# Kernel optimization log

Hardware: AMD Instinct MI355X
Metric: run time of the kernel (lower is better)

Reference implementation:

```python
import jax, jax.numpy as jnp
import numpy as np

ITE = 20
LAM = 0.1
MU1_0 = 0.1
MU2_0 = 0.1
RHO = 1.05


def _shrink(x, t):
    # soft-threshold: sign(x) * max(|x| - t, 0)
    return jnp.sign(x) * jnp.maximum(jnp.abs(x) - t, 0.0)


# circular forward differences (kernel [1, -1]) along W, H, and spectral (C) axes
def _diff_h(x):
    return x - jnp.roll(x, -1, axis=-1)

def _diff_v(x):
    return x - jnp.roll(x, -1, axis=-2)

def _diff_s(x):
    return x - jnp.roll(x, -1, axis=1)

# adjoint (transpose) differences used inside the FFT-based TV solve
def _diff_hT(x):
    return x - jnp.roll(x, 1, axis=-1)

def _diff_vT(x):
    return x - jnp.roll(x, 1, axis=-2)

def _diff_sT(x):
    return x - jnp.roll(x, 1, axis=1)


def _demo(C, H, W):
    # |F(Dh)|^2 + |F(Dv)|^2 + |F(Ds)|^2 for circular [1,-1] kernels:
    # |1 - exp(-2*pi*i*k/L)|^2 = 2 - 2*cos(2*pi*k/L) along each axis.
    dc = 2.0 - 2.0 * jnp.cos(2.0 * jnp.pi * jnp.arange(C) / C)
    dh = 2.0 - 2.0 * jnp.cos(2.0 * jnp.pi * jnp.arange(H) / H)
    dw = 2.0 - 2.0 * jnp.cos(2.0 * jnp.pi * jnp.arange(W) / W)
    return (dc[:, None, None] + dh[None, :, None] + dw[None, None, :]).astype(jnp.float32)  # [C,H,W]


def _hwtv3d(Y, inW):
    N, C, H, W = Y.shape
    demo = _demo(C, H, W)  # [C,H,W], broadcasts over batch
    mu1, mu2, lam = MU1_0, MU2_0, LAM
    zero = jnp.float32(0.0)
    G1 = G21 = G22 = G23 = zero  # scalar zeros, broadcast like the torch `0`
    Z = Y
    X = Y
    DhZ, DvZ, DsZ = _diff_h(Z), _diff_v(Z), _diff_s(Z)
    for _ in range(ITE):
        Uh = _shrink(DhZ - G21 / mu2, lam / mu2)
        Uv = _shrink(DvZ - G22 / mu2, lam / mu2)
        Us = _shrink(DsZ - G23 / mu2, lam / mu2)
        # TV_solver3D: (mu1*I + mu2*(Dh^T Dh + Dv^T Dv + Ds^T Ds))^{-1} applied via 3D FFT
        numer = mu1 * (X + G1 / mu1) + mu2 * (
            _diff_hT(Uh + G21 / mu2) + _diff_vT(Uv + G22 / mu2) + _diff_sT(Us + G23 / mu2)
        )
        F = jnp.fft.fftn(numer, axes=(1, 2, 3))
        Z = jnp.real(jnp.fft.ifftn(F / (mu1 + mu2 * demo), axes=(1, 2, 3)))
        DhZ, DvZ, DsZ = _diff_h(Z), _diff_v(Z), _diff_s(Z)
        X = (inW * Y + mu1 * Z - G1) / (inW + mu1)
        G1 = G1 + mu1 * (X - Z)
        G21 = G21 + mu2 * (Uh - DhZ)
        G22 = G22 + mu2 * (Uv - DvZ)
        G23 = G23 + mu2 * (Us - DsZ)
        mu1 = RHO * mu1
        mu2 = RHO * mu2
    return Z


def setup_inputs() -> dict:
    key = jax.random.key(0)
    k1, k2 = jax.random.split(key)
    Y = jax.random.normal(k1, (4, 31, 128, 128), dtype=jnp.float32)
    inW = jax.random.uniform(k2, (4, 31, 128, 128), dtype=jnp.float32)
    return {"Y": Y, "inW": inW}


def reference(Y, inW):
    return _hwtv3d(Y, inW)
```

## Files before the change

### kernel.cpp

```cpp
#include <hip/hip_runtime.h>
#include <hip/hip_fp16.h>
#include <math.h>

#define N_ 4
#define C_ 31
#define H_ 128
#define W_ 128
#define TOTAL (N_*C_*H_*W_)
#define CV_ (C_*H_*W_)
#define PI_F 3.14159265358979f
#define RHO_F 1.05f
#define INV_RHO (1.0f/1.05f)
#define NORM2 (1.0f/16384.0f)

typedef __attribute__((ext_vector_type(2))) float v2f;
typedef __attribute__((ext_vector_type(2))) _Float16 h2f;

__device__ __forceinline__ v2f cmulv(v2f a, v2f b){
  v2f t = a.x * b;
  v2f s = (v2f){-a.y, a.y};
  return t + s * b.yx;
}
__device__ __forceinline__ v2f shflv(v2f v, int m){
  v2f r; r.x = __shfl_xor(v.x, m, 64); r.y = __shfl_xor(v.y, m, 64); return r;
}
__device__ __forceinline__ h2f shflh(h2f v, int m){
  float f = __builtin_bit_cast(float, v);
  f = __shfl_xor(f, m, 64);
  return __builtin_bit_cast(h2f, f);
}
__device__ __forceinline__ float shrinkf(float x, float t){
  return copysignf(fmaxf(fabsf(x) - t, 0.0f), x);
}
__device__ __forceinline__ uint packh2(v2f v){
  union{__half2 h2; uint u;} cv; cv.h2 = __floats2half2_rn(v.x, v.y); return cv.u;
}
__device__ __forceinline__ v2f unpackh2(uint u){
  union{uint uu; __half2 h2;} cv; cv.uu = u;
  float2 f = __half22float2(cv.h2);
  return (v2f){f.x, f.y};
}
__device__ __forceinline__ v2f h2v(__half2 h){
  float2 f = __half22float2(h);
  return (v2f){f.x, f.y};
}
__device__ __forceinline__ v2f vupd(v2f D, v2f vo, float thr){
  const float aa = 1.0f + INV_RHO;
  return (v2f){
    shrinkf(aa*D.x - vo.x*INV_RHO, thr) + (vo.x - D.x)*INV_RHO,
    shrinkf(aa*D.y - vo.y*INV_RHO, thr) + (vo.y - D.y)*INV_RHO};
}
__device__ __forceinline__ void load_tw(const v2f* __restrict__ lut, v2f* tw, int lane){
  #pragma unroll
  for (int i = 0; i < 7; ++i) tw[i] = lut[i*64 + lane];
}

__device__ __forceinline__ void fft128_fwd(v2f& a, v2f& b, const v2f* twf, int t){
  v2f u = a + b;
  v2f v = cmulv(a - b, twf[0]);
  #pragma unroll
  for (int i = 1; i < 7; ++i){
    int sp = 64 >> i;
    bool up = (t & sp) != 0;
    v2f pu = shflv(u, sp);
    v2f du = up ? pu - u : u + pu;
    u = cmulv(du, twf[i]);
    v2f pv = shflv(v, sp);
    v2f dv = up ? pv - v : v + pv;
    v = cmulv(dv, twf[i]);
  }
  a = u; b = v;
}

__device__ __forceinline__ void fft128_inv(v2f& a, v2f& b, const v2f* twi, int t){
  v2f u = a, v = b;
  #pragma unroll
  for (int i = 6; i >= 1; --i){
    int sp = 64 >> i;
    bool up = (t & sp) != 0;
    v2f pu = shflv(u, sp);
    v2f e  = up ? pu : u;
    v2f o  = up ? u  : pu;
    v2f wo = cmulv(o, twi[i]);
    u = up ? e - wo : e + wo;
    v2f pv = shflv(v, sp);
    v2f ev = up ? pv : v;
    v2f ov = up ? v  : pv;
    v2f wv = cmulv(ov, twi[i]);
    v = up ? ev - wv : ev + wv;
  }
  v2f tv = cmulv(v, twi[0]);
  a = u + tv;
  b = u - tv;
}

__device__ __forceinline__ void fft128_inv_h2(h2f& are, h2f& aim, h2f& bre, h2f& bim,
    const uint* __restrict__ twc, const uint* __restrict__ tws, int t){
  #pragma unroll
  for (int i = 6; i >= 1; --i){
    int sp = 64 >> i;
    bool up = (t & sp) != 0;
    h2f c2 = __builtin_bit_cast(h2f, twc[i*64 + t]);
    h2f s2 = __builtin_bit_cast(h2f, tws[i*64 + t]);
    h2f pre = shflh(are, sp), pim = shflh(aim, sp);
    h2f e_re = up ? pre : are, e_im = up ? pim : aim;
    h2f o_re = up ? are : pre, o_im = up ? aim : pim;
    are = e_re + (o_re*c2 - o_im*s2);
    aim = e_im + (o_re*s2 + o_im*c2);
    pre = shflh(bre, sp); pim = shflh(bim, sp);
    e_re = up ? pre : bre; e_im = up ? pim : bim;
    o_re = up ? bre : pre; o_im = up ? bim : pim;
    bre = e_re + (o_re*c2 - o_im*s2);
    bim = e_im + (o_re*s2 + o_im*c2);
  }
  h2f c0 = __builtin_bit_cast(h2f, twc[t]);
  h2f s0 = __builtin_bit_cast(h2f, tws[t]);
  h2f tr = bre*c0 - bim*s0;
  h2f ti = bre*s0 + bim*c0;
  h2f ur = are, ui = aim;
  are = ur + tr; aim = ui + ti;
  bre = ur - tr; bim = ui - ti;
}

__device__ __forceinline__ void fft128_fwd_h2(h2f& are, h2f& aim, h2f& bre, h2f& bim,
    const uint* __restrict__ twc, const uint* __restrict__ tws, int t){
  h2f c0 = __builtin_bit_cast(h2f, twc[t]);
  h2f s0 = __builtin_bit_cast(h2f, tws[t]);
  h2f dre = are - bre, dim = aim - bim;
  h2f ure = are + bre, uim = aim + bim;
  h2f vre = dre*c0 - dim*s0;
  h2f vim = dre*s0 + dim*c0;
  #pragma unroll
  for (int i = 1; i < 7; ++i){
    int sp = 64 >> i;
    bool up = (t & sp) != 0;
    h2f c2 = __builtin_bit_cast(h2f, twc[i*64 + t]);
    h2f s2 = __builtin_bit_cast(h2f, tws[i*64 + t]);
    h2f sg = up ? (h2f){(_Float16)-1.0f, (_Float16)-1.0f} : (h2f){(_Float16)1.0f, (_Float16)1.0f};
    h2f pre = shflh(ure, sp), pim = shflh(uim, sp);
    h2f d1 = sg*ure + pre, d2 = sg*uim + pim;
    ure = d1*c2 - d2*s2; uim = d1*s2 + d2*c2;
    pre = shflh(vre, sp); pim = shflh(vim, sp);
    d1 = sg*vre + pre; d2 = sg*vim + pim;
    vre = d1*c2 - d2*s2; vim = d1*s2 + d2*c2;
  }
  are = ure; aim = uim; bre = vre; bim = vim;
}

__global__ __launch_bounds__(128) void kern_init(v2f* __restrict__ twf_lut,
    v2f* __restrict__ twi_lut, float* __restrict__ dtab,
    uint* __restrict__ twihc, uint* __restrict__ twihs,
    uint* __restrict__ twfhc, uint* __restrict__ twfhs)
{
  int t = threadIdx.x;
  if (t < 64){
    float s, c;
    sincosf(-2.0f*PI_F*(float)t/128.0f, &s, &c);
    twf_lut[t] = (v2f){c, s};
    { union{__half2 h; uint u;} cc, ss;
      cc.h = __floats2half2_rn(c, c); ss.h = __floats2half2_rn(s, s);
      twfhc[t] = cc.u; twfhs[t] = ss.u; }
    sincosf(+2.0f*PI_F*(float)t/128.0f, &s, &c);
    twi_lut[t] = (v2f){c, s};
    { union{__half2 h; uint u;} cc, ss;
      cc.h = __floats2half2_rn(c, c); ss.h = __floats2half2_rn(s, s);
      twihc[t] = cc.u; twihs[t] = ss.u; }
    #pragma unroll
    for (int i = 1; i < 7; ++i){
      int sp = 64 >> i;
      float angf = (t & sp) ? -2.0f*PI_F*(float)(t&(sp-1))/(float)(2*sp) : 0.0f;
      sincosf(angf, &s, &c);
      twf_lut[i*64 + t] = (v2f){c, s};
      { union{__half2 h; uint u;} cc, ss;
        cc.h = __floats2half2_rn(c, c); ss.h = __floats2half2_rn(s, s);
        twfhc[i*64 + t] = cc.u; twfhs[i*64 + t] = ss.u; }
      float angi = +2.0f*PI_F*(float)(t&(sp-1))/(float)(2*sp);
      sincosf(angi, &s, &c);
      twi_lut[i*64 + t] = (v2f){c, s};
      float ch = c, sh = s;
      if (t & sp){ ch = -ch; sh = -sh; }
      union{__half2 h; uint u;} cc, ss;
      cc.h = __floats2half2_rn(ch, ch); ss.h = __floats2half2_rn(sh, sh);
      twihc[i*64 + t] = cc.u; twihs[i*64 + t] = ss.u;
    }
  }
  dtab[t] = 2.0f - 2.0f*cosf(2.0f*PI_F*(float)t/128.0f);
}

__global__ __launch_bounds__(256) void kern_pack(const float* __restrict__ Y,
    const float* __restrict__ W, uint2* __restrict__ YWp)
{
  int i = blockIdx.x * 256 + threadIdx.x;
  int pair = i / CV_, j = i - pair*CV_;
  long b0 = (long)(2*pair)*CV_ + j, b1 = b0 + CV_;
  union{__half2 h2; uint u;} a, b;
  a.h2 = __floats2half2_rn(Y[b0], W[b0]);
  b.h2 = __floats2half2_rn(Y[b1], W[b1]);
  YWp[i] = make_uint2(a.u, b.u);
}

__global__ __launch_bounds__(256) void kern_fwd0(const float* __restrict__ Y,
    __half2* __restrict__ Vho, __half2* __restrict__ Vvo, __half2* __restrict__ Vso,
    __half2* __restrict__ A, float thr, const v2f* __restrict__ twf_lut)
{
  __shared__ v2f  zbuf[26][128];
  __shared__ uint zs[25][128];
  int tid = threadIdx.x, lane = tid & 63, wv = tid >> 6;
  int b = blockIdx.x;
  int ht = b & 15, c = (b >> 4) % C_, pair = b / (16*C_);
  int h0 = ht * 8;
  int cm1 = c ? c-1 : C_-1, cp1 = (c == C_-1) ? 0 : c+1;
  long v0 = (long)(2*pair)*CV_, v1 = v0 + CV_;

  for (int u = wv; u < 26; u += 4){
    int cc, h;
    if (u < 10){ cc = c; h = (h0 - 1 + u) & (H_-1); }
    else if (u < 18){ cc = cm1; h = h0 + u - 10; }
    else { cc = cp1; h = h0 + u - 18; }
    long rb = ((long)cc*H_ + h)*W_;
    #pragma unroll
    for (int e = 0; e < 2; ++e){
      int w = lane + 64*e;
      zbuf[u][w] = (v2f){Y[v0+rb+w], Y[v1+rb+w]};
    }
  }
  __syncthreads();

  v2f q[2][2], vs[2][2], vsm[2][2];
  #pragma unroll
  for (int r = 0; r < 2; ++r){
    int i = wv + 4*r, h = h0 + i;
    long pv = ((long)(pair*C_ + c)*H_ + h)*W_;
    #pragma unroll
    for (int e = 0; e < 2; ++e){
      int w = lane + 64*e;
      v2f z0 = zbuf[i+1][w];
      v2f zw = zbuf[i+1][(w+1)&(W_-1)];
      v2f zh = zbuf[i+2][w];
      v2f zc = zbuf[18+i][w];
      v2f zm = zbuf[10+i][w];
      v2f vh = (v2f){shrinkf(z0.x-zw.x,thr), shrinkf(z0.y-zw.y,thr)};
      v2f vv = (v2f){shrinkf(z0.x-zh.x,thr), shrinkf(z0.y-zh.y,thr)};
      v2f vsl= (v2f){shrinkf(z0.x-zc.x,thr), shrinkf(z0.y-zc.y,thr)};
      vsm[r][e] = (v2f){shrinkf(zm.x-z0.x,thr), shrinkf(zm.y-z0.y,thr)};
      Vho[pv+w] = __floats2half2_rn(vh.x, vh.y);
      Vvo[pv+w] = __floats2half2_rn(vv.x, vv.y);
      Vso[pv+w] = __floats2half2_rn(vsl.x, vsl.y);
      zs[i][w]   = packh2(vh);
      zs[9+i][w] = packh2(vv);
      vs[r][e] = vsl;
      q[r][e]  = z0;
    }
  }
  if (wv == 0){
    #pragma unroll
    for (int e = 0; e < 2; ++e){
      int w = lane + 64*e;
      v2f z0 = zbuf[0][w], zh = zbuf[1][w];
      v2f vvm = (v2f){shrinkf(z0.x-zh.x,thr), shrinkf(z0.y-zh.y,thr)};
      zs[8][w] = packh2(vvm);
    }
  }
  __syncthreads();

  v2f twf[7]; load_tw(twf_lut, twf, lane);
  #pragma unroll
  for (int r = 0; r < 2; ++r){
    int i = wv + 4*r;
    v2f nm[2];
    #pragma unroll
    for (int e = 0; e < 2; ++e){
      int w = lane + 64*e;
      v2f vh  = unpackh2(zs[i][w]);
      v2f vhm = unpackh2(zs[i][(w+W_-1)&(W_-1)]);
      v2f vv  = unpackh2(zs[9+i][w]);
      v2f vvm = unpackh2(zs[8+i][w]);
      nm[e] = q[r][e] + (vh - vhm) + (vv - vvm) + (vs[r][e] - vsm[r][e]);
    }
    fft128_fwd(nm[0], nm[1], twf, lane);
    zs[17+i][lane]    = packh2(nm[0]);
    zs[17+i][lane+64] = packh2(nm[1]);
  }
  __syncthreads();
  int4* A4 = (int4*)A;
  int p = tid >> 1, hq = tid & 1;
  union{int4 v; uint e[4];} u;
  #pragma unroll
  for (int j = 0; j < 4; ++j) u.e[j] = zs[17 + 4*hq + j][p];
  A4[((long)(pair*W_ + p)*C_ + c)*32 + 2*ht + hq] = u.v;
}

__global__ __launch_bounds__(1024) void kern_CH(__half2* __restrict__ A,
    const uint* __restrict__ twfhc, const uint* __restrict__ twfhs,
    const uint* __restrict__ twihc, const uint* __restrict__ twihs,
    const float* __restrict__ dtab)
{
  __shared__ v2f slab[C_][H_];
  __shared__ v2f slab2[C_][H_];
  int tid = threadIdx.x, lane = tid & 63, wv = tid >> 6;
  int bid = blockIdx.x;
  int w = bid & (W_-1);
  const int4* g4 = (const int4*)(A + (long)bid * C_ * H_);

  if (tid < 992){
    union { int4 v; __half2 e[4]; } u;
    u.v = g4[tid];
    int c = tid >> 5, hb = (tid & 31) << 2;
    #pragma unroll
    for (int j = 0; j < 4; ++j) slab[c][hb+j] = h2v(u.e[j]);
  }
  __syncthreads();

  {
    int c1 = wv, c2 = (wv + 16 < C_) ? wv + 16 : (C_-1);
    v2f a0 = slab[c1][lane], b0 = slab[c1][lane+64];
    v2f a1 = slab[c2][lane], b1 = slab[c2][lane+64];
    h2f are = (h2f){(_Float16)a0.x, (_Float16)a1.x};
    h2f aim = (h2f){(_Float16)a0.y, (_Float16)a1.y};
    h2f bre = (h2f){(_Float16)b0.x, (_Float16)b1.x};
    h2f bim = (h2f){(_Float16)b0.y, (_Float16)b1.y};
    fft128_fwd_h2(are, aim, bre, bim, twfhc, twfhs, lane);
    slab[c1][lane]    = (v2f){(float)are.x, (float)aim.x};
    slab[c1][lane+64] = (v2f){(float)bre.x, (float)bim.x};
    if (wv + 16 < C_){
      slab[c2][lane]    = (v2f){(float)are.y, (float)aim.y};
      slab[c2][lane+64] = (v2f){(float)bre.y, (float)bim.y};
    }
  }
  __syncthreads();

  {
    int col = tid & (H_-1), cb = tid >> 7, c0 = cb * 4;
    int fh = __brev(col) >> 25;
    int fw = __brev(w)   >> 25;
    float beta = 1.0f + dtab[fh] + dtab[fw];
    float a2 = beta + 2.0f;
    float s  = sqrtf(a2*a2 - 4.0f);
    float rg = (a2 - s) * 0.5f;
    float gt[9];
    gt[0] = NORM2 / s;
    #pragma unroll
    for (int t = 1; t < 9; ++t) gt[t] = gt[t-1] * rg;

    v2f win[20];
    #pragma unroll
    for (int i = 0; i < 20; ++i){
      int ci = c0 - 8 + i;
      if (ci < 0) ci += C_;
      if (ci >= C_) ci -= C_;
      win[i] = slab[ci][col];
    }
    #pragma unroll
    for (int j = 0; j < 4; ++j){
      v2f o = (v2f){0.0f, 0.0f};
      #pragma unroll
      for (int t = -8; t <= 8; ++t){
        float gv = gt[t < 0 ? -t : t];
        o += gv * win[j + 8 - t];
      }
      int c = c0 + j;
      if (c < C_) slab2[c][col] = o;
    }
  }
  __syncthreads();

  {
    int c1 = wv, c2 = (wv + 16 < C_) ? wv + 16 : (C_-1);
    v2f a0 = slab2[c1][lane], b0 = slab2[c1][lane+64];
    v2f a1 = slab2[c2][lane], b1 = slab2[c2][lane+64];
    h2f are = (h2f){(_Float16)a0.x, (_Float16)a1.x};
    h2f aim = (h2f){(_Float16)a0.y, (_Float16)a1.y};
    h2f bre = (h2f){(_Float16)b0.x, (_Float16)b1.x};
    h2f bim = (h2f){(_Float16)b0.y, (_Float16)b1.y};
    fft128_inv_h2(are, aim, bre, bim, twihc, twihs, lane);
    slab2[c1][lane]    = (v2f){(float)are.x, (float)aim.x};
    slab2[c1][lane+64] = (v2f){(float)bre.x, (float)bim.x};
    if (wv + 16 < C_){
      slab2[c2][lane]    = (v2f){(float)are.y, (float)aim.y};
      slab2[c2][lane+64] = (v2f){(float)bre.y, (float)bim.y};
    }
  }
  __syncthreads();
  int4* go4 = (int4*)(A + (long)bid * C_ * H_);
  if (tid < 992){
    int c = tid >> 5, hb = (tid & 31) << 2;
    union { int4 v; __half2 e[4]; } u;
    #pragma unroll
    for (int j = 0; j < 4; ++j){
      v2f f = slab2[c][hb+j];
      u.e[j] = __floats2half2_rn(f.x, f.y);
    }
    go4[tid] = u.v;
  }
}

__global__ __launch_bounds__(512,4) void kern_CA(
    const __half2* __restrict__ Ain, __half2* __restrict__ Aout,
    const __half2* __restrict__ Vhi, const __half2* __restrict__ Vvi, const __half2* __restrict__ Vsi,
    __half2* __restrict__ Vho, __half2* __restrict__ Vvo, __half2* __restrict__ Vso,
    const uint2* __restrict__ YWp, __half2* __restrict__ G1,
    float mu, float thrn, float invmun, int firstG,
    const uint* __restrict__ twfhc, const uint* __restrict__ twfhs,
    const uint* __restrict__ twihc, const uint* __restrict__ twihs)
{
  __shared__ v2f  zbuf[36][128];
  __shared__ uint zs[50][128];
  int tid = threadIdx.x, lane = tid & 63, wv = tid >> 6;
  int b = blockIdx.x;
  int ht = b & 15, ct = (b >> 4) & 15, pair = b >> 8;
  int c0 = 2*ct, nc = (ct == 15) ? 1 : 2;
  int h0 = ht * 8;
  int cm1 = c0 ? c0-1 : C_-1;
  int cp  = (c0 + nc) % C_;

  int h = h0 + wv;
  long pv0 = ((long)(pair*C_ + c0)*H_ + h)*W_;
  long pv1 = ((long)(pair*C_ + ((nc==2)?c0+1:c0))*H_ + h)*W_;
  long pvm = ((long)(pair*C_ + cm1)*H_ + h)*W_;
  uint pf_vh[2][2], pf_vv[2][2], pf_vs[2][2], pf_vsm0[2], pf_g1[2][2], pf_vvh[2];
  uint2 pf_yw[2][2];
  #pragma unroll
  for (int e = 0; e < 2; ++e){
    int w = lane + 64*e;
    pf_vh[0][e] = *(const uint*)(Vhi + pv0 + w);
    pf_vh[1][e] = *(const uint*)(Vhi + pv1 + w);
    pf_vv[0][e] = *(const uint*)(Vvi + pv0 + w);
    pf_vv[1][e] = *(const uint*)(Vvi + pv1 + w);
    pf_vs[0][e] = *(const uint*)(Vsi + pv0 + w);
    pf_vs[1][e] = *(const uint*)(Vsi + pv1 + w);
    pf_vsm0[e]  = *(const uint*)(Vsi + pvm + w);
    pf_yw[0][e] = YWp[pv0 + w];
    pf_yw[1][e] = YWp[pv1 + w];
    pf_g1[0][e] = *(const uint*)(G1 + pv0 + w);
    pf_g1[1][e] = *(const uint*)(G1 + pv1 + w);
  }
  if (wv < 2){
    int cc = (wv == 0) ? c0 : ((nc==2)? c0+1 : c0);
    long pvh = ((long)(pair*C_ + cc)*H_ + ((h0+H_-1)&(H_-1)))*W_;
    #pragma unroll
    for (int e = 0; e < 2; ++e){
      int w = lane + 64*e;
      pf_vvh[e] = *(const uint*)(Vvi + pvh + w);
    }
  }

  const int4* A4 = (const int4*)Ain;
  #pragma unroll
  for (int k = 0; k < 3; ++k){
    int s = tid + 512*k;
    int q = s >> 7, w = s & 127;
    int cc, hq;
    if (q < 4){ cc = c0; hq = (2*ht - 1 + q) & 31; }
    else if (q < 8){ cc = (nc==2) ? c0+1 : c0; hq = (2*ht - 1 + (q-4)) & 31; }
    else if (q < 10){ cc = cm1; hq = 2*ht + (q-8); }
    else { cc = cp; hq = 2*ht + (q-10); }
    union{int4 v; uint e[4];} u;
    u.v = A4[((long)(pair*W_ + w)*C_ + cc)*32 + hq];
    #pragma unroll
    for (int j = 0; j < 4; ++j) zs[4*q + j][w] = u.e[j];
  }
  __syncthreads();

  {
    int uu_[5], zr_[5];
    #pragma unroll
    for (int k = 0; k < 5; ++k){
      int uu = wv + 8*k;
      int zr;
      if (uu < 10) zr = 3 + uu;
      else if (uu < 20) zr = 19 + (uu - 10);
      else if (uu < 28) zr = 32 + (uu - 20);
      else if (uu < 36) zr = 40 + (uu - 28);
      else zr = 0;
      uu_[k] = uu; zr_[k] = zr;
    }
    #pragma unroll
    for (int p = 0; p < 3; ++p){
      int kP = 2*p, kQ = (p < 2) ? (2*p+1) : 2*p;
      uint r0a = zs[zr_[kP]][lane],    r1a = zs[zr_[kQ]][lane];
      uint r0b = zs[zr_[kP]][lane+64], r1b = zs[zr_[kQ]][lane+64];
      h2f are = __builtin_bit_cast(h2f, (r0a & 0xffffu) | (r1a << 16));
      h2f aim = __builtin_bit_cast(h2f, (r0a >> 16) | (r1a & 0xffff0000u));
      h2f bre = __builtin_bit_cast(h2f, (r0b & 0xffffu) | (r1b << 16));
      h2f bim = __builtin_bit_cast(h2f, (r0b >> 16) | (r1b & 0xffff0000u));
      fft128_inv_h2(are, aim, bre, bim, twihc, twihs, lane);
      if (p < 2){
        zbuf[uu_[kP]][lane]    = (v2f){(float)are.x, (float)aim.x};
        zbuf[uu_[kP]][lane+64] = (v2f){(float)bre.x, (float)bim.x};
        zbuf[uu_[kQ]][lane]    = (v2f){(float)are.y, (float)aim.y};
        zbuf[uu_[kQ]][lane+64] = (v2f){(float)bre.y, (float)bim.y};
      } else if (uu_[4] < 36){
        zbuf[uu_[4]][lane]     = (v2f){(float)are.x, (float)aim.x};
        zbuf[uu_[4]][lane+64]  = (v2f){(float)bre.x, (float)bim.x};
      }
    }
  }
  __syncthreads();

  v2f q2[2][2], vs2[2][2], vsm2[2][2];
  #pragma unroll
  for (int s = 0; s < 2; ++s){
    if (s == 1 && nc == 1) break;
    int rr = wv + 8*s;
    int zb0 = (s == 0) ? (1 + wv) : (11 + wv);
    int zbc = (s == 0) ? ((nc==2) ? (11 + wv) : (28 + wv)) : (28 + wv);
    int zbm = (s == 0) ? (20 + wv) : (1 + wv);
    long pv = (s == 0) ? pv0 : pv1;
    #pragma unroll
    for (int e = 0; e < 2; ++e){
      int w = lane + 64*e;
      v2f z0 = zbuf[zb0][w];
      v2f zw = zbuf[zb0][(w+1)&(W_-1)];
      v2f zh = zbuf[zb0+1][w];
      v2f zc = zbuf[zbc][w];
      v2f zm = zbuf[zbm][w];
      v2f vh  = vupd(z0 - zw, unpackh2(pf_vh[s][e]), thrn);
      v2f vv  = vupd(z0 - zh, unpackh2(pf_vv[s][e]), thrn);
      v2f vsl = vupd(z0 - zc, unpackh2(pf_vs[s][e]), thrn);
      if (s == 0){
        vsm2[0][e] = vupd(zm - z0, unpackh2(pf_vsm0[e]), thrn);
        vsm2[1][e] = vsl;
      }
      Vho[pv+w] = __floats2half2_rn(vh.x, vh.y);
      Vvo[pv+w] = __floats2half2_rn(vv.x, vv.y);
      Vso[pv+w] = __floats2half2_rn(vsl.x, vsl.y);
      zs[rr][w]    = packh2(vh);
      zs[16+rr][w] = packh2(vv);
      vs2[s][e] = vsl;
      v2f a0 = unpackh2(pf_yw[s][e].x);
      v2f a1 = unpackh2(pf_yw[s][e].y);
      v2f g1 = firstG ? (v2f){0.0f, 0.0f} : unpackh2(pf_g1[s][e]);
      float x0 = (a0.y*a0.x + mu*z0.x - g1.x) * __builtin_amdgcn_rcpf(a0.y + mu);
      float x1 = (a1.y*a1.x + mu*z0.y - g1.y) * __builtin_amdgcn_rcpf(a1.y + mu);
      float g10 = g1.x + mu*(x0 - z0.x);
      float g11 = g1.y + mu*(x1 - z0.y);
      G1[pv+w] = __floats2half2_rn(g10, g11);
      q2[s][e] = (v2f){x0 + g10*invmun, x1 + g11*invmun};
    }
  }
  if (wv < 2 && !(wv == 1 && nc == 1)){
    int zb = (wv == 0) ? 0 : 10;
    #pragma unroll
    for (int e = 0; e < 2; ++e){
      int w = lane + 64*e;
      v2f z0 = zbuf[zb][w], zh = zbuf[zb+1][w];
      v2f vvm = vupd(z0 - zh, unpackh2(pf_vvh[e]), thrn);
      zs[32+wv][w] = packh2(vvm);
    }
  }
  __syncthreads();

  {
    v2f nm[2][2];
    #pragma unroll
    for (int s = 0; s < 2; ++s){
      int rr = wv + 8*s;
      #pragma unroll
      for (int e = 0; e < 2; ++e){
        int w = lane + 64*e;
        v2f vh  = unpackh2(zs[rr][w]);
        v2f vhm = unpackh2(zs[rr][(w+W_-1)&(W_-1)]);
        v2f vv  = unpackh2(zs[16+rr][w]);
        v2f vvm = (wv == 0) ? unpackh2(zs[32+s][w]) : unpackh2(zs[16+rr-1][w]);
        nm[s][e] = q2[s][e] + (vh - vhm) + (vv - vvm) + (vs2[s][e] - vsm2[s][e]);
      }
    }
    if (nc == 1){ nm[1][0] = nm[0][0]; nm[1][1] = nm[0][1]; }
    h2f are = (h2f){(_Float16)nm[0][0].x, (_Float16)nm[1][0].x};
    h2f aim = (h2f){(_Float16)nm[0][0].y, (_Float16)nm[1][0].y};
    h2f bre = (h2f){(_Float16)nm[0][1].x, (_Float16)nm[1][1].x};
    h2f bim = (h2f){(_Float16)nm[0][1].y, (_Float16)nm[1][1].y};
    fft128_fwd_h2(are, aim, bre, bim, twfhc, twfhs, lane);
    uint a_ = __builtin_bit_cast(uint, are), ai_ = __builtin_bit_cast(uint, aim);
    uint b_ = __builtin_bit_cast(uint, bre), bi_ = __builtin_bit_cast(uint, bim);
    zs[34+wv][lane]    = (a_ & 0xffffu) | (ai_ << 16);
    zs[34+wv][lane+64] = (b_ & 0xffffu) | (bi_ << 16);
    if (nc == 2){
      zs[42+wv][lane]    = (a_ >> 16) | (ai_ & 0xffff0000u);
      zs[42+wv][lane+64] = (b_ >> 16) | (bi_ & 0xffff0000u);
    }
  }
  __syncthreads();

  {
    int q = tid >> 7, w = tid & 127;
    int cL = q >> 1, hq2 = q & 1;
    if (cL < nc){
      int4* Ao4 = (int4*)Aout;
      union{int4 v; uint e[4];} uo;
      #pragma unroll
      for (int j = 0; j < 4; ++j) uo.e[j] = zs[34 + 8*cL + 4*hq2 + j][w];
      Ao4[((long)(pair*W_ + w)*C_ + (c0+cL))*32 + 2*ht + hq2] = uo.v;
    }
  }
}

__global__ __launch_bounds__(256) void kern_last(const __half2* __restrict__ A,
    float* __restrict__ Z, const v2f* __restrict__ twi_lut)
{
  __shared__ uint zs[8][128];
  int tid = threadIdx.x, lane = tid & 63, wv = tid >> 6;
  int b = blockIdx.x;
  int ht = b & 15, c = (b >> 4) % C_, pair = b / (16*C_);
  int h0 = ht * 8;
  const int4* A4 = (const int4*)A;
  {
    int p = tid >> 1, hq = tid & 1;
    union{int4 v; uint e[4];} u;
    u.v = A4[((long)(pair*W_ + p)*C_ + c)*32 + 2*ht + hq];
    #pragma unroll
    for (int j = 0; j < 4; ++j) zs[4*hq + j][p] = u.e[j];
  }
  __syncthreads();
  v2f twi[7]; load_tw(twi_lut, twi, lane);
  long v0 = (long)(2*pair)*CV_, v1 = v0 + CV_;
  #pragma unroll
  for (int r = 0; r < 2; ++r){
    int i = wv + 4*r, h = h0 + i;
    v2f a = unpackh2(zs[i][lane]);
    v2f bb = unpackh2(zs[i][lane+64]);
    fft128_inv(a, bb, twi, lane);
    long rb = ((long)c*H_ + h)*W_;
    Z[v0+rb+lane]    = a.x;  Z[v1+rb+lane]    = a.y;
    Z[v0+rb+lane+64] = bb.x; Z[v1+rb+lane+64] = bb.y;
  }
}

extern "C" void kernel_launch(void* const* d_in, const int* in_sizes, int n_in,
                              void* d_out, int out_size, void* d_ws, size_t ws_size,
                              hipStream_t stream)
{
  const float* Y   = (const float*)d_in[0];
  const float* inW = (const float*)d_in[1];
  float* Z = (float*)d_out;

  v2f*   twf_lut = (v2f*)d_ws;
  v2f*   twi_lut = twf_lut + 7*64;
  float* dtab    = (float*)(twi_lut + 7*64);
  uint*  twihc   = (uint*)(dtab + 128);
  uint*  twihs   = twihc + 7*64;
  uint*  twfhc   = twihs + 7*64;
  uint*  twfhs   = twfhc + 7*64;
  char*  fields  = (char*)d_ws + 16384;

  const int HT = TOTAL/2;
  uint2*   YWp = (uint2*)fields;
  __half2* G1  = (__half2*)(YWp + HT);
  __half2* Vh0 = G1  + HT;
  __half2* Vv0 = Vh0 + HT;
  __half2* Vs0 = Vv0 + HT;
  __half2* Vh1 = Vs0 + HT;
  __half2* Vv1 = Vh1 + HT;
  __half2* Vs1 = Vv1 + HT;
  __half2* A0  = Vs1 + HT;
  __half2* A1  = A0  + HT;
  __half2* Vh[2] = {Vh0, Vh1};
  __half2* Vv[2] = {Vv0, Vv1};
  __half2* Vs[2] = {Vs0, Vs1};
  __half2* Ab[2] = {A0, A1};

  kern_init<<<dim3(1), dim3(128), 0, stream>>>(twf_lut, twi_lut, dtab, twihc, twihs, twfhc, twfhs);
  kern_pack<<<dim3(2*CV_/256), dim3(256), 0, stream>>>(Y, inW, YWp);
  kern_fwd0<<<dim3(2*C_*16), dim3(256), 0, stream>>>(Y, Vh0, Vv0, Vs0, A0, 1.0f, twf_lut);

  float mu = 0.1f;
  for (int t = 0; t < 19; ++t){
    kern_CH<<<dim3(2*W_), dim3(1024), 0, stream>>>(Ab[t&1], twfhc, twfhs, twihc, twihs, dtab);
    float mun = mu * RHO_F;
    kern_CA<<<dim3(512), dim3(512), 0, stream>>>(
        Ab[t&1], Ab[(t+1)&1],
        Vh[t&1], Vv[t&1], Vs[t&1],
        Vh[(t+1)&1], Vv[(t+1)&1], Vs[(t+1)&1],
        YWp, G1, mu, 0.1f/mun, 1.0f/mun, (t==0) ? 1 : 0,
        twfhc, twfhs, twihc, twihs);
    mu = mun;
  }
  kern_CH<<<dim3(2*W_), dim3(1024), 0, stream>>>(Ab[1], twfhc, twfhs, twihc, twihs, dtab);
  kern_last<<<dim3(2*C_*16), dim3(256), 0, stream>>>(Ab[1], Z, twi_lut);
}
```

Baseline: 537.6 us.

## Process four channels per block in kern_CA to cut halo reloads

kern_CA now covers four spectral channels per block with 1024 threads instead of two channels with 512, halving the grid to 256 blocks. Neighbouring-channel and H-halo rows loaded from A and inverse-FFT'd are shared across more channels, so less redundant global traffic and FFT work is spent on halos. The cost is larger shared memory use (zbuf and zs grow) and fewer, bigger blocks, which lowers occupancy and the number of blocks per CU. The last block handles three channels via validity masks.

```diff
diff --git a/kernel.cpp b/kernel.cpp
--- a/kernel.cpp
+++ b/kernel.cpp
@@ -394,7 +394,7 @@
   }
 }
 
-__global__ __launch_bounds__(512,4) void kern_CA(
+__global__ __launch_bounds__(1024) void kern_CA(
     const __half2* __restrict__ Ain, __half2* __restrict__ Aout,
     const __half2* __restrict__ Vhi, const __half2* __restrict__ Vvi, const __half2* __restrict__ Vsi,
     __half2* __restrict__ Vho, __half2* __restrict__ Vvo, __half2* __restrict__ Vso,
@@ -403,39 +403,43 @@
     const uint* __restrict__ twfhc, const uint* __restrict__ twfhs,
     const uint* __restrict__ twihc, const uint* __restrict__ twihs)
 {
-  __shared__ v2f  zbuf[36][128];
-  __shared__ uint zs[50][128];
+  __shared__ v2f  zbuf[56][128];
+  __shared__ uint zs[80][128];
   int tid = threadIdx.x, lane = tid & 63, wv = tid >> 6;
   int b = blockIdx.x;
-  int ht = b & 15, ct = (b >> 4) & 15, pair = b >> 8;
-  int c0 = 2*ct, nc = (ct == 15) ? 1 : 2;
+  int ht = b & 15, ct = (b >> 4) & 7, pair = b >> 7;
+  int c0 = 4*ct, nc = (ct == 7) ? 3 : 4;
   int h0 = ht * 8;
+  int k = wv >> 3, hl = wv & 7;
   int cm1 = c0 ? c0-1 : C_-1;
-  int cp  = (c0 + nc) % C_;
-
-  int h = h0 + wv;
-  long pv0 = ((long)(pair*C_ + c0)*H_ + h)*W_;
-  long pv1 = ((long)(pair*C_ + ((nc==2)?c0+1:c0))*H_ + h)*W_;
-  long pvm = ((long)(pair*C_ + cm1)*H_ + h)*W_;
-  uint pf_vh[2][2], pf_vv[2][2], pf_vs[2][2], pf_vsm0[2], pf_g1[2][2], pf_vvh[2];
+  int cp4 = (c0 + 4) % C_;
+
+  int cA = c0 + 2*k;
+  int cB = (c0 + 2*k + 1) % C_;
+  int cAm1 = cA ? cA-1 : C_-1;
+  int h = h0 + hl;
+  long pvA = ((long)(pair*C_ + cA)*H_ + h)*W_;
+  long pvB = ((long)(pair*C_ + cB)*H_ + h)*W_;
+  long pvM = ((long)(pair*C_ + cAm1)*H_ + h)*W_;
+  uint pf_vh[2][2], pf_vv[2][2], pf_vs[2][2], pf_vsmA[2], pf_g1[2][2], pf_vvh[2];
   uint2 pf_yw[2][2];
   #pragma unroll
   for (int e = 0; e < 2; ++e){
     int w = lane + 64*e;
-    pf_vh[0][e] = *(const uint*)(Vhi + pv0 + w);
-    pf_vh[1][e] = *(const uint*)(Vhi + pv1 + w);
-    pf_vv[0][e] = *(const uint*)(Vvi + pv0 + w);
-    pf_vv[1][e] = *(const uint*)(Vvi + pv1 + w);
-    pf_vs[0][e] = *(const uint*)(Vsi + pv0 + w);
-    pf_vs[1][e] = *(const uint*)(Vsi + pv1 + w);
-    pf_vsm0[e]  = *(const uint*)(Vsi + pvm + w);
-    pf_yw[0][e] = YWp[pv0 + w];
-    pf_yw[1][e] = YWp[pv1 + w];
-    pf_g1[0][e] = *(const uint*)(G1 + pv0 + w);
-    pf_g1[1][e] = *(const uint*)(G1 + pv1 + w);
-  }
-  if (wv < 2){
-    int cc = (wv == 0) ? c0 : ((nc==2)? c0+1 : c0);
+    pf_vh[0][e] = *(const uint*)(Vhi + pvA + w);
+    pf_vh[1][e] = *(const uint*)(Vhi + pvB + w);
+    pf_vv[0][e] = *(const uint*)(Vvi + pvA + w);
+    pf_vv[1][e] = *(const uint*)(Vvi + pvB + w);
+    pf_vs[0][e] = *(const uint*)(Vsi + pvA + w);
+    pf_vs[1][e] = *(const uint*)(Vsi + pvB + w);
+    pf_vsmA[e]  = *(const uint*)(Vsi + pvM + w);
+    pf_yw[0][e] = YWp[pvA + w];
+    pf_yw[1][e] = YWp[pvB + w];
+    pf_g1[0][e] = *(const uint*)(G1 + pvA + w);
+    pf_g1[1][e] = *(const uint*)(G1 + pvB + w);
+  }
+  if (wv < 4){
+    int cc = (c0 + wv) % C_;
     long pvh = ((long)(pair*C_ + cc)*H_ + ((h0+H_-1)&(H_-1)))*W_;
     #pragma unroll
     for (int e = 0; e < 2; ++e){
@@ -446,53 +450,47 @@
 
   const int4* A4 = (const int4*)Ain;
   #pragma unroll
-  for (int k = 0; k < 3; ++k){
-    int s = tid + 512*k;
-    int q = s >> 7, w = s & 127;
-    int cc, hq;
-    if (q < 4){ cc = c0; hq = (2*ht - 1 + q) & 31; }
-    else if (q < 8){ cc = (nc==2) ? c0+1 : c0; hq = (2*ht - 1 + (q-4)) & 31; }
-    else if (q < 10){ cc = cm1; hq = 2*ht + (q-8); }
-    else { cc = cp; hq = 2*ht + (q-10); }
-    union{int4 v; uint e[4];} u;
-    u.v = A4[((long)(pair*W_ + w)*C_ + cc)*32 + hq];
-    #pragma unroll
-    for (int j = 0; j < 4; ++j) zs[4*q + j][w] = u.e[j];
+  for (int kk = 0; kk < 3; ++kk){
+    int s = tid + 1024*kk;
+    if (s < 2560){
+      int qq = s >> 7, w = s & 127;
+      int cc, hq, base;
+      if (qq < 16){
+        cc = (c0 + (qq >> 2)) % C_;
+        hq = (2*ht - 1 + (qq & 3)) & 31;
+        base = (qq >> 2)*16 + (qq & 3)*4;
+      } else if (qq < 18){
+        cc = cm1; hq = 2*ht + (qq - 16); base = 64 + (qq - 16)*4;
+      } else {
+        cc = cp4; hq = 2*ht + (qq - 18); base = 72 + (qq - 18)*4;
+      }
+      union{int4 v; uint e[4];} u;
+      u.v = A4[((long)(pair*W_ + w)*C_ + cc)*32 + hq];
+      #pragma unroll
+      for (int j = 0; j < 4; ++j) zs[base+j][w] = u.e[j];
+    }
   }
   __syncthreads();
 
   {
-    int uu_[5], zr_[5];
-    #pragma unroll
-    for (int k = 0; k < 5; ++k){
-      int uu = wv + 8*k;
-      int zr;
-      if (uu < 10) zr = 3 + uu;
-      else if (uu < 20) zr = 19 + (uu - 10);
-      else if (uu < 28) zr = 32 + (uu - 20);
-      else if (uu < 36) zr = 40 + (uu - 28);
-      else zr = 0;
-      uu_[k] = uu; zr_[k] = zr;
-    }
-    #pragma unroll
-    for (int p = 0; p < 3; ++p){
-      int kP = 2*p, kQ = (p < 2) ? (2*p+1) : 2*p;
-      uint r0a = zs[zr_[kP]][lane],    r1a = zs[zr_[kQ]][lane];
-      uint r0b = zs[zr_[kP]][lane+64], r1b = zs[zr_[kQ]][lane+64];
+    #pragma unroll
+    for (int kk = 0; kk < 2; ++kk){
+      int j = wv + 16*kk;
+      if (kk == 1 && j >= 28) break;
+      int bP = 2*j, bQ = 2*j + 1;
+      int zrP = (bP < 40) ? ((bP/10)*16 + (bP%10) + 3) : (bP + 24);
+      int zrQ = (bQ < 40) ? ((bQ/10)*16 + (bQ%10) + 3) : (bQ + 24);
+      uint r0a = zs[zrP][lane],    r1a = zs[zrQ][lane];
+      uint r0b = zs[zrP][lane+64], r1b = zs[zrQ][lane+64];
       h2f are = __builtin_bit_cast(h2f, (r0a & 0xffffu) | (r1a << 16));
       h2f aim = __builtin_bit_cast(h2f, (r0a >> 16) | (r1a & 0xffff0000u));
       h2f bre = __builtin_bit_cast(h2f, (r0b & 0xffffu) | (r1b << 16));
       h2f bim = __builtin_bit_cast(h2f, (r0b >> 16) | (r1b & 0xffff0000u));
       fft128_inv_h2(are, aim, bre, bim, twihc, twihs, lane);
-      if (p < 2){
-        zbuf[uu_[kP]][lane]    = (v2f){(float)are.x, (float)aim.x};
-        zbuf[uu_[kP]][lane+64] = (v2f){(float)bre.x, (float)bim.x};
-        zbuf[uu_[kQ]][lane]    = (v2f){(float)are.y, (float)aim.y};
-        zbuf[uu_[kQ]][lane+64] = (v2f){(float)bre.y, (float)bim.y};
-      } else if (uu_[4] < 36){
-        zbuf[uu_[4]][lane]     = (v2f){(float)are.x, (float)aim.x};
-        zbuf[uu_[4]][lane+64]  = (v2f){(float)bre.x, (float)bim.x};
-      }
+      zbuf[bP][lane]    = (v2f){(float)are.x, (float)aim.x};
+      zbuf[bP][lane+64] = (v2f){(float)bre.x, (float)bim.x};
+      zbuf[bQ][lane]    = (v2f){(float)are.y, (float)aim.y};
+      zbuf[bQ][lane+64] = (v2f){(float)bre.y, (float)bim.y};
     }
   }
   __syncthreads();
@@ -500,12 +498,12 @@
   v2f q2[2][2], vs2[2][2], vsm2[2][2];
   #pragma unroll
   for (int s = 0; s < 2; ++s){
-    if (s == 1 && nc == 1) break;
-    int rr = wv + 8*s;
-    int zb0 = (s == 0) ? (1 + wv) : (11 + wv);
-    int zbc = (s == 0) ? ((nc==2) ? (11 + wv) : (28 + wv)) : (28 + wv);
-    int zbm = (s == 0) ? (20 + wv) : (1 + wv);
-    long pv = (s == 0) ? pv0 : pv1;
+    int cL = 2*k + s;
+    bool valid = (cL < nc);
+    int zb0 = 10*cL + 1 + hl;
+    int zbc = (cL < 3) ? (10*(cL+1) + 1 + hl) : (48 + hl);
+    int zbm = (cL == 0) ? (40 + hl) : (10*(cL-1) + 1 + hl);
+    long pv = (s == 0) ? pvA : pvB;
     #pragma unroll
     for (int e = 0; e < 2; ++e){
       int w = lane + 64*e;
@@ -513,19 +511,21 @@
       v2f zw = zbuf[zb0][(w+1)&(W_-1)];
       v2f zh = zbuf[zb0+1][w];
       v2f zc = zbuf[zbc][w];
-      v2f zm = zbuf[zbm][w];
       v2f vh  = vupd(z0 - zw, unpackh2(pf_vh[s][e]), thrn);
       v2f vv  = vupd(z0 - zh, unpackh2(pf_vv[s][e]), thrn);
       v2f vsl = vupd(z0 - zc, unpackh2(pf_vs[s][e]), thrn);
       if (s == 0){
-        vsm2[0][e] = vupd(zm - z0, unpackh2(pf_vsm0[e]), thrn);
+        v2f zm = zbuf[zbm][w];
+        vsm2[0][e] = vupd(zm - z0, unpackh2(pf_vsmA[e]), thrn);
         vsm2[1][e] = vsl;
       }
-      Vho[pv+w] = __floats2half2_rn(vh.x, vh.y);
-      Vvo[pv+w] = __floats2half2_rn(vv.x, vv.y);
-      Vso[pv+w] = __floats2half2_rn(vsl.x, vsl.y);
-      zs[rr][w]    = packh2(vh);
-      zs[16+rr][w] = packh2(vv);
+      if (valid){
+        Vho[pv+w] = __floats2half2_rn(vh.x, vh.y);
+        Vvo[pv+w] = __floats2half2_rn(vv.x, vv.y);
+        Vso[pv+w] = __floats2half2_rn(vsl.x, vsl.y);
+      }
+      zs[cL*8 + hl][w]      = packh2(vh);
+      zs[32 + cL*8 + hl][w] = packh2(vv);
       vs2[s][e] = vsl;
       v2f a0 = unpackh2(pf_yw[s][e].x);
       v2f a1 = unpackh2(pf_yw[s][e].y);
@@ -534,18 +534,18 @@
       float x1 = (a1.y*a1.x + mu*z0.y - g1.y) * __builtin_amdgcn_rcpf(a1.y + mu);
       float g10 = g1.x + mu*(x0 - z0.x);
       float g11 = g1.y + mu*(x1 - z0.y);
-      G1[pv+w] = __floats2half2_rn(g10, g11);
+      if (valid) G1[pv+w] = __floats2half2_rn(g10, g11);
       q2[s][e] = (v2f){x0 + g10*invmun, x1 + g11*invmun};
     }
   }
-  if (wv < 2 && !(wv == 1 && nc == 1)){
-    int zb = (wv == 0) ? 0 : 10;
+  if (wv < 4){
+    int zb = 10*wv;
     #pragma unroll
     for (int e = 0; e < 2; ++e){
       int w = lane + 64*e;
       v2f z0 = zbuf[zb][w], zh = zbuf[zb+1][w];
       v2f vvm = vupd(z0 - zh, unpackh2(pf_vvh[e]), thrn);
-      zs[32+wv][w] = packh2(vvm);
+      zs[64 + wv][w] = packh2(vvm);
     }
   }
   __syncthreads();
@@ -554,18 +554,19 @@
     v2f nm[2][2];
     #pragma unroll
     for (int s = 0; s < 2; ++s){
-      int rr = wv + 8*s;
+      int cL = 2*k + s;
       #pragma unroll
       for (int e = 0; e < 2; ++e){
         int w = lane + 64*e;
-        v2f vh  = unpackh2(zs[rr][w]);
-        v2f vhm = unpackh2(zs[rr][(w+W_-1)&(W_-1)]);
-        v2f vv  = unpackh2(zs[16+rr][w]);
-        v2f vvm = (wv == 0) ? unpackh2(zs[32+s][w]) : unpackh2(zs[16+rr-1][w]);
+        v2f vh  = unpackh2(zs[cL*8 + hl][w]);
+        v2f vhm = unpackh2(zs[cL*8 + hl][(w+W_-1)&(W_-1)]);
+        v2f vv  = unpackh2(zs[32 + cL*8 + hl][w]);
+        v2f vvm = (hl == 0) ? unpackh2(zs[64 + cL][w]) : unpackh2(zs[32 + cL*8 + hl - 1][w]);
         nm[s][e] = q2[s][e] + (vh - vhm) + (vv - vvm) + (vs2[s][e] - vsm2[s][e]);
       }
     }
-    if (nc == 1){ nm[1][0] = nm[0][0]; nm[1][1] = nm[0][1]; }
+    bool validB = (2*k + 1 < nc);
+    if (!validB){ nm[1][0] = nm[0][0]; nm[1][1] = nm[0][1]; }
     h2f are = (h2f){(_Float16)nm[0][0].x, (_Float16)nm[1][0].x};
     h2f aim = (h2f){(_Float16)nm[0][0].y, (_Float16)nm[1][0].y};
     h2f bre = (h2f){(_Float16)nm[0][1].x, (_Float16)nm[1][1].x};
@@ -573,11 +574,13 @@
     fft128_fwd_h2(are, aim, bre, bim, twfhc, twfhs, lane);
     uint a_ = __builtin_bit_cast(uint, are), ai_ = __builtin_bit_cast(uint, aim);
     uint b_ = __builtin_bit_cast(uint, bre), bi_ = __builtin_bit_cast(uint, bim);
-    zs[34+wv][lane]    = (a_ & 0xffffu) | (ai_ << 16);
-    zs[34+wv][lane+64] = (b_ & 0xffffu) | (bi_ << 16);
-    if (nc == 2){
-      zs[42+wv][lane]    = (a_ >> 16) | (ai_ & 0xffff0000u);
-      zs[42+wv][lane+64] = (b_ >> 16) | (bi_ & 0xffff0000u);
+    uint* tb = (uint*)zbuf;
+    int r0 = (2*k)*8 + hl, r1 = (2*k+1)*8 + hl;
+    tb[r0*128 + lane]      = (a_ & 0xffffu) | (ai_ << 16);
+    tb[r0*128 + lane + 64] = (b_ & 0xffffu) | (bi_ << 16);
+    if (validB){
+      tb[r1*128 + lane]      = (a_ >> 16) | (ai_ & 0xffff0000u);
+      tb[r1*128 + lane + 64] = (b_ >> 16) | (bi_ & 0xffff0000u);
     }
   }
   __syncthreads();
@@ -586,10 +589,11 @@
     int q = tid >> 7, w = tid & 127;
     int cL = q >> 1, hq2 = q & 1;
     if (cL < nc){
+      const uint* tb = (const uint*)zbuf;
       int4* Ao4 = (int4*)Aout;
       union{int4 v; uint e[4];} uo;
       #pragma unroll
-      for (int j = 0; j < 4; ++j) uo.e[j] = zs[34 + 8*cL + 4*hq2 + j][w];
+      for (int j = 0; j < 4; ++j) uo.e[j] = tb[(cL*8 + 4*hq2 + j)*128 + w];
       Ao4[((long)(pair*W_ + w)*C_ + (c0+cL))*32 + 2*ht + hq2] = uo.v;
     }
   }
@@ -667,7 +671,7 @@
   for (int t = 0; t < 19; ++t){
     kern_CH<<<dim3(2*W_), dim3(1024), 0, stream>>>(Ab[t&1], twfhc, twfhs, twihc, twihs, dtab);
     float mun = mu * RHO_F;
-    kern_CA<<<dim3(512), dim3(512), 0, stream>>>(
+    kern_CA<<<dim3(256), dim3(1024), 0, stream>>>(
         Ab[t&1], Ab[(t+1)&1],
         Vh[t&1], Vv[t&1], Vs[t&1],
         Vh[(t+1)&1], Vv[(t+1)&1], Vs[(t+1)&1],
```

Result: faster. 523.6 us (median of 3 runs) (-2.6%).
